# Performance work log

Measured on AMD Instinct MI355X. Metric: run time of the kernel, lower is better.

The kernel has to match this reference:

```python
import jax, jax.numpy as jnp
import numpy as np

B, C, D, H, W = 4, 128, 16, 16, 16
INNER = 64  # channels // reduction


def setup_inputs() -> dict:
    key = jax.random.key(0)
    ks = jax.random.split(key, 4)
    s = 0.02
    return {
        "x": jax.random.normal(ks[0], (B, C, D, H, W), dtype=jnp.float32),
        "Wq": jax.random.normal(ks[1], (INNER, C), dtype=jnp.float32) * s,
        "bq": jnp.zeros((INNER,), dtype=jnp.float32),
        "Wk": jax.random.normal(ks[2], (INNER, C), dtype=jnp.float32) * s,
        "bk": jnp.zeros((INNER,), dtype=jnp.float32),
        "Wv": jax.random.normal(ks[3], (C, C), dtype=jnp.float32) * s,
        "bv": jnp.zeros((C,), dtype=jnp.float32),
        "gamma": jnp.zeros((1,), dtype=jnp.float32),
    }


def reference(x, Wq, bq, Wk, bk, Wv, bv, gamma):
    b, c, d, h, w = x.shape
    n = d * h * w
    inner = Wq.shape[0]
    scale = inner ** (-0.5)
    xf = x.reshape(b, c, n)  # flatten spatial dims
    # 1x1 Conv3d == per-position channel matmul
    q = jnp.einsum('oc,bcn->bon', Wq, xf) + bq[None, :, None]  # [B, inner, N]
    k = jnp.einsum('oc,bcn->bon', Wk, xf) + bk[None, :, None]  # [B, inner, N]
    v = jnp.einsum('oc,bcn->bon', Wv, xf) + bv[None, :, None]  # [B, C, N]
    # attn[b, n, m] = softmax_m(q[:, :, n] . k[:, :, m] * scale)
    attn = jax.nn.softmax(jnp.einsum('bon,bom->bnm', q, k) * scale, axis=-1)
    # out = v @ attn^T  -> out[b, c, n] = sum_m v[b, c, m] * attn[b, n, m]
    out = jnp.einsum('bcm,bnm->bcn', v, attn).reshape(b, c, d, h, w)
    return x + gamma[0] * out
```

## Files before the change

kernel.cpp:

```cpp
#include <hip/hip_runtime.h>
#include <cstdint>

#define B_ 4
#define C_ 128
#define INNER_ 64
#define N_ 4096
#define S_ 4
#define KEYS_PER_BLOCK (N_ / S_)
#define KT 64
#define NT (KEYS_PER_BLOCK / KT)

typedef __attribute__((ext_vector_type(8))) short short8;
typedef __attribute__((ext_vector_type(4))) float f32x4;

typedef const __attribute__((address_space(1))) void* gp_t;
typedef __attribute__((address_space(3))) void* lp_t;

__device__ __forceinline__ short f2bf(float f) {
  unsigned u = __builtin_bit_cast(unsigned, f);
  unsigned r = (u + 0x7FFFu + ((u >> 16) & 1u)) >> 16;
  return (short)r;
}

__global__ __launch_bounds__(256) void pack_kernel(
    const float* __restrict__ Wq, const float* __restrict__ bq,
    const float* __restrict__ Wk, const float* __restrict__ bk,
    const float* __restrict__ Wv, const float* __restrict__ bv,
    short* __restrict__ wp, float* __restrict__ bp)
{
  const int idx = blockIdx.x * 256 + threadIdx.x;
  const int o = idx >> 7, c = idx & 127;
  float v;
  if (o < 64)       v = Wq[o * C_ + c];
  else if (o < 128) v = Wk[(o - 64) * C_ + c];
  else              v = Wv[(o - 128) * C_ + c];
  wp[idx] = f2bf(v);
  if (c == 0)
    bp[o] = (o < 64) ? bq[o] : (o < 128) ? bk[o - 64] : bv[o - 128];
}

__global__ __launch_bounds__(256) void qkv_kernel(
    const float* __restrict__ x, const short* __restrict__ wp,
    const float* __restrict__ bp,
    short* __restrict__ qb, short* __restrict__ kb, short* __restrict__ vb)
{
  __shared__ short xT[16 * 136];
  const int tid = threadIdx.x;
  const int b   = blockIdx.x >> 8;
  const int n0  = (blockIdx.x & 255) << 4;

  const float* xb = x + (size_t)b * C_ * N_ + n0;
  for (int i = tid; i < 512; i += 256) {
    const int c = i >> 2, seg = i & 3;
    const float4 v = *(const float4*)&xb[(size_t)c * N_ + seg * 4];
    xT[(seg * 4 + 0) * 136 + c] = f2bf(v.x);
    xT[(seg * 4 + 1) * 136 + c] = f2bf(v.y);
    xT[(seg * 4 + 2) * 136 + c] = f2bf(v.z);
    xT[(seg * 4 + 3) * 136 + c] = f2bf(v.w);
  }
  __syncthreads();

  const int w = tid >> 6, lane = tid & 63, quad = lane >> 4, l16 = lane & 15;

#pragma unroll
  for (int oi = 0; oi < 4; ++oi) {
    const int ot = w + oi * 4;
    const int o  = ot * 16 + l16;

    short8 bf[4];
#pragma unroll
    for (int ks = 0; ks < 4; ++ks)
      bf[ks] = *(const short8*)&wp[(size_t)o * 128 + ks * 32 + quad * 8];

    f32x4 acc = (f32x4){0.f, 0.f, 0.f, 0.f};
#pragma unroll
    for (int ks = 0; ks < 4; ++ks) {
      short8 af = *(const short8*)&xT[l16 * 136 + ks * 32 + quad * 8];
      acc = __builtin_amdgcn_mfma_f32_16x16x32_bf16(af, bf[ks], acc, 0, 0, 0);
    }

    const float bias = bp[o];
#pragma unroll
    for (int r = 0; r < 4; ++r) {
      const int n = n0 + quad * 4 + r;
      const short sv = f2bf(acc[r] + bias);
      if (o < 64)       qb[((size_t)b * N_ + n) * 64 + o] = sv;
      else if (o < 128) kb[((size_t)b * N_ + n) * 64 + (o - 64)] = sv;
      else              vb[((size_t)b * C_ + (o - 128)) * N_ + n] = sv;
    }
  }
}

__global__ __launch_bounds__(256) void attn_kernel(
    const short* __restrict__ qb, const short* __restrict__ kb,
    const short* __restrict__ vb,
    float* __restrict__ Opart, float* __restrict__ lbuf)
{
  __shared__ short kbuf[2][4096];
  __shared__ short vbuf[2][8192];
  __shared__ short parena[4][2048];

  const int tid = threadIdx.x;
  const int bid = blockIdx.x;
  const int b   = bid >> 7;
  const int qt  = (bid >> 2) & 31;
  const int s   = bid & 3;
  const int m0  = qt << 7;
  const int w   = tid >> 6, lane = tid & 63, quad = lane >> 4, l16 = lane & 15;
  const int rbase = m0 + w * 32;

  short* pw = parena[w];

  const float kS = 0.125f * 1.44269504088896340736f;

  short8 qa[2][2];
#pragma unroll
  for (int mt = 0; mt < 2; ++mt)
#pragma unroll
    for (int kk = 0; kk < 2; ++kk)
      qa[mt][kk] = *(const short8*)&qb[((size_t)b * N_ + rbase + mt * 16 + l16) * 64 + kk * 32 + quad * 8];

  float lsum[2][4];
#pragma unroll
  for (int mt = 0; mt < 2; ++mt)
#pragma unroll
    for (int r = 0; r < 4; ++r) lsum[mt][r] = 0.f;
  f32x4 accO[2][8];
#pragma unroll
  for (int mt = 0; mt < 2; ++mt)
#pragma unroll
    for (int ct = 0; ct < 8; ++ct) accO[mt][ct] = (f32x4){0.f, 0.f, 0.f, 0.f};

  const int kslice = s * KEYS_PER_BLOCK;

  auto dma_tile = [&](int kt, int d) {
    const int kbase = kslice + kt * KT;
#pragma unroll
    for (int t = 0; t < 2; ++t) {
      const int p = (w * 2 + t) * 64 + lane;
      const int key = p >> 3, jm = (p & 7) ^ (key & 7);
      const short* src = kb + (((size_t)b * N_ + kbase + key) << 6) + jm * 8;
      __builtin_amdgcn_global_load_lds((gp_t)src, (lp_t)&kbuf[d][(w * 2 + t) * 512], 16, 0, 0);
    }
#pragma unroll
    for (int t = 0; t < 4; ++t) {
      const int p = (w * 4 + t) * 64 + lane;
      const int ch = p >> 3, jm = (p & 7) ^ (ch & 7);
      const short* src = vb + ((size_t)b * C_ + ch) * N_ + kbase + jm * 8;
      __builtin_amdgcn_global_load_lds((gp_t)src, (lp_t)&vbuf[d][(w * 4 + t) * 512], 16, 0, 0);
    }
  };

  dma_tile(0, 0);

  for (int kt = 0; kt < NT; ++kt) {
    __syncthreads();
    if (kt + 1 < NT) dma_tile(kt + 1, (kt + 1) & 1);
    const int d = kt & 1;

#pragma unroll
    for (int ct = 0; ct < 4; ++ct) {
      short8 kf[2];
#pragma unroll
      for (int kk = 0; kk < 2; ++kk)
        kf[kk] = *(const short8*)&kbuf[d][((ct * 16 + l16) << 6) + (((kk * 4 + quad) ^ (l16 & 7)) << 3)];
      f32x4 s0 = (f32x4){0.f, 0.f, 0.f, 0.f};
      f32x4 s1 = (f32x4){0.f, 0.f, 0.f, 0.f};
      s0 = __builtin_amdgcn_mfma_f32_16x16x32_bf16(qa[0][0], kf[0], s0, 0, 0, 0);
      s0 = __builtin_amdgcn_mfma_f32_16x16x32_bf16(qa[0][1], kf[1], s0, 0, 0, 0);
      s1 = __builtin_amdgcn_mfma_f32_16x16x32_bf16(qa[1][0], kf[0], s1, 0, 0, 0);
      s1 = __builtin_amdgcn_mfma_f32_16x16x32_bf16(qa[1][1], kf[1], s1, 0, 0, 0);

      const int jp = ct * 2 + (l16 >> 3);
      const int off = l16 & 7;
#pragma unroll
      for (int r = 0; r < 4; ++r) {
        const int row0 = quad * 4 + r;
        const float p0 = exp2f(s0[r] * kS);
        lsum[0][r] += p0;
        pw[(row0 << 6) + ((jp ^ (row0 & 7)) << 3) + off] = f2bf(p0);
        const float p1 = exp2f(s1[r] * kS);
        lsum[1][r] += p1;
        pw[((16 + row0) << 6) + ((jp ^ (row0 & 7)) << 3) + off] = f2bf(p1);
      }
    }

#pragma unroll
    for (int ks = 0; ks < 2; ++ks) {
      short8 pa0 = *(const short8*)&pw[(l16 << 6) + (((ks * 4 + quad) ^ (l16 & 7)) << 3)];
      short8 pa1 = *(const short8*)&pw[((16 + l16) << 6) + (((ks * 4 + quad) ^ (l16 & 7)) << 3)];
#pragma unroll
      for (int ct = 0; ct < 8; ++ct) {
        short8 vf = *(const short8*)&vbuf[d][((ct * 16 + l16) << 6) + (((ks * 4 + quad) ^ (l16 & 7)) << 3)];
        accO[0][ct] = __builtin_amdgcn_mfma_f32_16x16x32_bf16(pa0, vf, accO[0][ct], 0, 0, 0);
        accO[1][ct] = __builtin_amdgcn_mfma_f32_16x16x32_bf16(pa1, vf, accO[1][ct], 0, 0, 0);
      }
    }
  }

#pragma unroll
  for (int mt = 0; mt < 2; ++mt) {
#pragma unroll
    for (int r = 0; r < 4; ++r) {
      lsum[mt][r] += __shfl_xor(lsum[mt][r], 1);
      lsum[mt][r] += __shfl_xor(lsum[mt][r], 2);
      lsum[mt][r] += __shfl_xor(lsum[mt][r], 4);
      lsum[mt][r] += __shfl_xor(lsum[mt][r], 8);
    }
    if (l16 == 0) {
#pragma unroll
      for (int r = 0; r < 4; ++r)
        lbuf[((size_t)b * S_ + s) * N_ + rbase + mt * 16 + quad * 4 + r] = lsum[mt][r];
    }
#pragma unroll
    for (int ct = 0; ct < 8; ++ct) {
#pragma unroll
      for (int r = 0; r < 4; ++r) {
        const int n = rbase + mt * 16 + quad * 4 + r;
        Opart[(((size_t)b * S_ + s) * N_ + n) * C_ + ct * 16 + l16] = accO[mt][ct][r];
      }
    }
  }
}

__global__ __launch_bounds__(256) void combine_kernel(
    const float* __restrict__ x, const float* __restrict__ gamma,
    const float* __restrict__ Opart, const float* __restrict__ lbuf,
    float* __restrict__ out)
{
  __shared__ float Of[32][133];
  __shared__ float Linv[32];

  const int t  = threadIdx.x;
  const int b  = blockIdx.x >> 7;
  const int n0 = (blockIdx.x & 127) << 5;

  const int c4 = (t & 31) * 4, nrow = t >> 5;
#pragma unroll
  for (int np = 0; np < 4; ++np) {
    const int n = np * 8 + nrow;
    f32x4 acc = (f32x4){0.f, 0.f, 0.f, 0.f};
#pragma unroll
    for (int sp = 0; sp < S_; ++sp) {
      const f32x4 v = *(const f32x4*)&Opart[(((size_t)b * S_ + sp) * N_ + n0 + n) * C_ + c4];
      acc += v;
    }
    Of[n][c4 + 0] = acc[0];
    Of[n][c4 + 1] = acc[1];
    Of[n][c4 + 2] = acc[2];
    Of[n][c4 + 3] = acc[3];
  }
  if (t < 32) {
    float L = 0.f;
#pragma unroll
    for (int sp = 0; sp < S_; ++sp) L += lbuf[((size_t)b * S_ + sp) * N_ + n0 + t];
    Linv[t] = 1.f / L;
  }
  __syncthreads();

  const float g = gamma[0];
  const int nn = t & 31, cb = t >> 5;
#pragma unroll
  for (int cp = 0; cp < 16; ++cp) {
    const int c = cp * 8 + cb;
    const size_t idx = ((size_t)b * C_ + c) * N_ + n0 + nn;
    out[idx] = x[idx] + g * Of[nn][c] * Linv[nn];
  }
}

extern "C" void kernel_launch(void* const* d_in, const int* in_sizes, int n_in,
                              void* d_out, int out_size, void* d_ws, size_t ws_size,
                              hipStream_t stream) {
  const float* x     = (const float*)d_in[0];
  const float* Wq    = (const float*)d_in[1];
  const float* bq    = (const float*)d_in[2];
  const float* Wk    = (const float*)d_in[3];
  const float* bk    = (const float*)d_in[4];
  const float* Wv    = (const float*)d_in[5];
  const float* bv    = (const float*)d_in[6];
  const float* gamma = (const float*)d_in[7];
  float* out = (float*)d_out;

  short* qb = (short*)d_ws;
  short* kb = qb + (size_t)B_ * N_ * INNER_;
  short* vb = kb + (size_t)B_ * N_ * INNER_;
  float* Opart = (float*)(vb + (size_t)B_ * C_ * N_);
  float* lbuf  = Opart + (size_t)B_ * S_ * N_ * C_;
  float* bp    = lbuf + (size_t)B_ * S_ * N_;
  short* wp    = (short*)(bp + 256);

  pack_kernel<<<128, 256, 0, stream>>>(Wq, bq, Wk, bk, Wv, bv, wp, bp);
  qkv_kernel<<<B_ * (N_ / 16), 256, 0, stream>>>(x, wp, bp, qb, kb, vb);
  attn_kernel<<<B_ * (N_ / 128) * S_, 256, 0, stream>>>(qb, kb, vb, Opart, lbuf);
  combine_kernel<<<B_ * (N_ / 32), 256, 0, stream>>>(x, gamma, Opart, lbuf, out);
}
```

Measured before the change: 143.9 us.

## Rework attention pipeline: register-resident P, bf16 partials, more key splits

The attention kernel now computes transposed scores (K·Q) so the bf16 probabilities stay in registers and feed 16x16x16 MFMAs directly, which removes the LDS round trip for P. Key splits double from 4 to 8 and launch bounds request 3 blocks per CU for more parallelism. Partial outputs are stored as bf16 in channel-major layout, so combine can read them vectorized, and a separate kernel precomputes the inverse row sums. The QKV projection now handles 32 positions per block and stages results in LDS for coalesced 16-byte stores. The costs are lower precision in the partial sums, twice as much partial data to reduce, and one extra kernel launch.

```diff
diff --git a/kernel.cpp b/kernel.cpp
--- a/kernel.cpp
+++ b/kernel.cpp
@@ -5,12 +5,13 @@
 #define C_ 128
 #define INNER_ 64
 #define N_ 4096
-#define S_ 4
+#define S_ 8
 #define KEYS_PER_BLOCK (N_ / S_)
 #define KT 64
 #define NT (KEYS_PER_BLOCK / KT)
 
 typedef __attribute__((ext_vector_type(8))) short short8;
+typedef __attribute__((ext_vector_type(4))) short bf16x4;
 typedef __attribute__((ext_vector_type(4))) float f32x4;
 
 typedef const __attribute__((address_space(1))) void* gp_t;
@@ -20,6 +21,22 @@
   unsigned u = __builtin_bit_cast(unsigned, f);
   unsigned r = (u + 0x7FFFu + ((u >> 16) & 1u)) >> 16;
   return (short)r;
+}
+__device__ __forceinline__ float bf2f(short s) {
+  return __builtin_bit_cast(float, ((unsigned)(unsigned short)s) << 16);
+}
+
+__device__ __forceinline__ f32x4 mfma16(bf16x4 a, bf16x4 b, f32x4 c) {
+#if __has_builtin(__builtin_amdgcn_mfma_f32_16x16x16bf16_1k)
+  return __builtin_amdgcn_mfma_f32_16x16x16bf16_1k(a, b, c, 0, 0, 0);
+#elif __has_builtin(__builtin_amdgcn_mfma_f32_16x16x16_bf16)
+  return __builtin_amdgcn_mfma_f32_16x16x16_bf16(a, b, c, 0, 0, 0);
+#else
+  f32x4 d;
+  asm volatile("v_mfma_f32_16x16x16_bf16 %0, %1, %2, %3"
+               : "=v"(d) : "v"(a), "v"(b), "v"(c));
+  return d;
+#endif
 }
 
 __global__ __launch_bounds__(256) void pack_kernel(
@@ -42,16 +59,20 @@
 __global__ __launch_bounds__(256) void qkv_kernel(
     const float* __restrict__ x, const short* __restrict__ wp,
     const float* __restrict__ bp,
-    short* __restrict__ qb, short* __restrict__ kb, short* __restrict__ vb)
-{
-  __shared__ short xT[16 * 136];
+    short* __restrict__ qg, short* __restrict__ kg, short* __restrict__ vg)
+{
+  __shared__ short xT[32 * 136];
+  __shared__ short outb[256 * 40];
+  __shared__ float biasL[256];
+
   const int tid = threadIdx.x;
-  const int b   = blockIdx.x >> 8;
-  const int n0  = (blockIdx.x & 255) << 4;
-
+  const int b   = blockIdx.x >> 7;
+  const int n0  = (blockIdx.x & 127) << 5;
+
+  biasL[tid] = bp[tid];
   const float* xb = x + (size_t)b * C_ * N_ + n0;
-  for (int i = tid; i < 512; i += 256) {
-    const int c = i >> 2, seg = i & 3;
+  for (int i = tid; i < 1024; i += 256) {
+    const int c = i >> 3, seg = i & 7;
     const float4 v = *(const float4*)&xb[(size_t)c * N_ + seg * 4];
     xT[(seg * 4 + 0) * 136 + c] = f2bf(v.x);
     xT[(seg * 4 + 1) * 136 + c] = f2bf(v.y);
@@ -62,55 +83,96 @@
 
   const int w = tid >> 6, lane = tid & 63, quad = lane >> 4, l16 = lane & 15;
 
-#pragma unroll
-  for (int oi = 0; oi < 4; ++oi) {
-    const int ot = w + oi * 4;
-    const int o  = ot * 16 + l16;
-
-    short8 bf[4];
-#pragma unroll
-    for (int ks = 0; ks < 4; ++ks)
-      bf[ks] = *(const short8*)&wp[(size_t)o * 128 + ks * 32 + quad * 8];
-
-    f32x4 acc = (f32x4){0.f, 0.f, 0.f, 0.f};
-#pragma unroll
-    for (int ks = 0; ks < 4; ++ks) {
-      short8 af = *(const short8*)&xT[l16 * 136 + ks * 32 + quad * 8];
-      acc = __builtin_amdgcn_mfma_f32_16x16x32_bf16(af, bf[ks], acc, 0, 0, 0);
-    }
-
-    const float bias = bp[o];
-#pragma unroll
-    for (int r = 0; r < 4; ++r) {
-      const int n = n0 + quad * 4 + r;
-      const short sv = f2bf(acc[r] + bias);
-      if (o < 64)       qb[((size_t)b * N_ + n) * 64 + o] = sv;
-      else if (o < 128) kb[((size_t)b * N_ + n) * 64 + (o - 64)] = sv;
-      else              vb[((size_t)b * C_ + (o - 128)) * N_ + n] = sv;
-    }
-  }
-}
-
-__global__ __launch_bounds__(256) void attn_kernel(
+  short8 xf[2][4];
+#pragma unroll
+  for (int nt = 0; nt < 2; ++nt)
+#pragma unroll
+    for (int kk = 0; kk < 4; ++kk)
+      xf[nt][kk] = *(const short8*)&xT[(nt * 16 + l16) * 136 + kk * 32 + quad * 8];
+
+  if (w < 2) {
+    const int obase = w * 64;
+#pragma unroll
+    for (int ot = 0; ot < 4; ++ot) {
+      const int o = obase + ot * 16 + l16;
+      short8 wf[4];
+#pragma unroll
+      for (int kk = 0; kk < 4; ++kk)
+        wf[kk] = *(const short8*)&wp[(size_t)o * 128 + kk * 32 + quad * 8];
+      const float bias = biasL[o];
+#pragma unroll
+      for (int nt = 0; nt < 2; ++nt) {
+        f32x4 acc = (f32x4){0.f, 0.f, 0.f, 0.f};
+#pragma unroll
+        for (int kk = 0; kk < 4; ++kk)
+          acc = __builtin_amdgcn_mfma_f32_16x16x32_bf16(xf[nt][kk], wf[kk], acc, 0, 0, 0);
+#pragma unroll
+        for (int r = 0; r < 4; ++r)
+          outb[o * 40 + nt * 16 + quad * 4 + r] = f2bf(acc[r] + bias);
+      }
+    }
+  } else {
+    const int ob2 = (w - 2) * 64;
+#pragma unroll
+    for (int ot = 0; ot < 4; ++ot) {
+      const int orow = 128 + ob2 + ot * 16 + l16;
+      short8 wf[4];
+#pragma unroll
+      for (int kk = 0; kk < 4; ++kk)
+        wf[kk] = *(const short8*)&wp[(size_t)orow * 128 + kk * 32 + quad * 8];
+#pragma unroll
+      for (int nt = 0; nt < 2; ++nt) {
+        f32x4 acc = (f32x4){0.f, 0.f, 0.f, 0.f};
+#pragma unroll
+        for (int kk = 0; kk < 4; ++kk)
+          acc = __builtin_amdgcn_mfma_f32_16x16x32_bf16(wf[kk], xf[nt][kk], acc, 0, 0, 0);
+#pragma unroll
+        for (int r = 0; r < 4; ++r) {
+          const int o_r = 128 + ob2 + ot * 16 + quad * 4 + r;
+          outb[o_r * 40 + nt * 16 + l16] = f2bf(acc[r] + biasL[o_r]);
+        }
+      }
+    }
+  }
+  __syncthreads();
+
+  {
+    const int n = tid >> 3, oc = tid & 7;
+    short8 qv, kv;
+#pragma unroll
+    for (int j = 0; j < 8; ++j) {
+      qv[j] = outb[(oc * 8 + j) * 40 + n];
+      kv[j] = outb[(64 + oc * 8 + j) * 40 + n];
+    }
+    *(short8*)&qg[(((size_t)b * N_ + n0 + n) << 6) + oc * 8] = qv;
+    *(short8*)&kg[(((size_t)b * N_ + n0 + n) << 6) + oc * 8] = kv;
+#pragma unroll
+    for (int rep = 0; rep < 2; ++rep) {
+      const int idx2 = tid + rep * 256;
+      const int orel = idx2 >> 2, nc = idx2 & 3;
+      const short8 vv = *(const short8*)&outb[(128 + orel) * 40 + nc * 8];
+      *(short8*)&vg[(((size_t)b * C_ + orel) << 12) + n0 + nc * 8] = vv;
+    }
+  }
+}
+
+__global__ __launch_bounds__(256, 3) void attn_kernel(
     const short* __restrict__ qb, const short* __restrict__ kb,
     const short* __restrict__ vb,
-    float* __restrict__ Opart, float* __restrict__ lbuf)
+    short* __restrict__ Opart, float* __restrict__ lbuf)
 {
   __shared__ short kbuf[2][4096];
   __shared__ short vbuf[2][8192];
-  __shared__ short parena[4][2048];
 
   const int tid = threadIdx.x;
   const int bid = blockIdx.x;
-  const int b   = bid >> 7;
-  const int qt  = (bid >> 2) & 31;
-  const int s   = bid & 3;
+  const int b   = bid >> 8;
+  const int qt  = (bid >> 3) & 31;
+  const int s   = bid & 7;
   const int m0  = qt << 7;
   const int w   = tid >> 6, lane = tid & 63, quad = lane >> 4, l16 = lane & 15;
   const int rbase = m0 + w * 32;
 
-  short* pw = parena[w];
-
   const float kS = 0.125f * 1.44269504088896340736f;
 
   short8 qa[2][2];
@@ -120,16 +182,12 @@
     for (int kk = 0; kk < 2; ++kk)
       qa[mt][kk] = *(const short8*)&qb[((size_t)b * N_ + rbase + mt * 16 + l16) * 64 + kk * 32 + quad * 8];
 
-  float lsum[2][4];
-#pragma unroll
-  for (int mt = 0; mt < 2; ++mt)
-#pragma unroll
-    for (int r = 0; r < 4; ++r) lsum[mt][r] = 0.f;
-  f32x4 accO[2][8];
-#pragma unroll
-  for (int mt = 0; mt < 2; ++mt)
-#pragma unroll
-    for (int ct = 0; ct < 8; ++ct) accO[mt][ct] = (f32x4){0.f, 0.f, 0.f, 0.f};
+  float lsum[2] = {0.f, 0.f};
+  f32x4 accO[8][2];
+#pragma unroll
+  for (int vt = 0; vt < 8; ++vt)
+#pragma unroll
+    for (int mt = 0; mt < 2; ++mt) accO[vt][mt] = (f32x4){0.f, 0.f, 0.f, 0.f};
 
   const int kslice = s * KEYS_PER_BLOCK;
 
@@ -158,114 +216,107 @@
     if (kt + 1 < NT) dma_tile(kt + 1, (kt + 1) & 1);
     const int d = kt & 1;
 
+    bf16x4 pbf[4][2];
 #pragma unroll
     for (int ct = 0; ct < 4; ++ct) {
-      short8 kf[2];
-#pragma unroll
-      for (int kk = 0; kk < 2; ++kk)
-        kf[kk] = *(const short8*)&kbuf[d][((ct * 16 + l16) << 6) + (((kk * 4 + quad) ^ (l16 & 7)) << 3)];
-      f32x4 s0 = (f32x4){0.f, 0.f, 0.f, 0.f};
-      f32x4 s1 = (f32x4){0.f, 0.f, 0.f, 0.f};
-      s0 = __builtin_amdgcn_mfma_f32_16x16x32_bf16(qa[0][0], kf[0], s0, 0, 0, 0);
-      s0 = __builtin_amdgcn_mfma_f32_16x16x32_bf16(qa[0][1], kf[1], s0, 0, 0, 0);
-      s1 = __builtin_amdgcn_mfma_f32_16x16x32_bf16(qa[1][0], kf[0], s1, 0, 0, 0);
-      s1 = __builtin_amdgcn_mfma_f32_16x16x32_bf16(qa[1][1], kf[1], s1, 0, 0, 0);
-
-      const int jp = ct * 2 + (l16 >> 3);
-      const int off = l16 & 7;
+      const short8 kf0 = *(const short8*)&kbuf[d][((ct * 16 + l16) << 6) + ((quad ^ (l16 & 7)) << 3)];
+      const short8 kf1 = *(const short8*)&kbuf[d][((ct * 16 + l16) << 6) + (((4 + quad) ^ (l16 & 7)) << 3)];
+#pragma unroll
+      for (int mt = 0; mt < 2; ++mt) {
+        f32x4 st = (f32x4){0.f, 0.f, 0.f, 0.f};
+        st = __builtin_amdgcn_mfma_f32_16x16x32_bf16(kf0, qa[mt][0], st, 0, 0, 0);
+        st = __builtin_amdgcn_mfma_f32_16x16x32_bf16(kf1, qa[mt][1], st, 0, 0, 0);
+        bf16x4 p4;
+#pragma unroll
+        for (int r = 0; r < 4; ++r) {
+          const float p = exp2f(st[r] * kS);
+          lsum[mt] += p;
+          p4[r] = f2bf(p);
+        }
+        pbf[ct][mt] = p4;
+      }
+    }
+
+#pragma unroll
+    for (int vt = 0; vt < 8; ++vt) {
+#pragma unroll
+      for (int ct = 0; ct < 4; ++ct) {
+        const int chunk = ct * 2 + (quad >> 1);
+        const bf16x4 vf = *(const bf16x4*)&vbuf[d][((vt * 16 + l16) << 6) +
+                              ((chunk ^ (l16 & 7)) << 3) + ((quad & 1) << 2)];
+        accO[vt][0] = mfma16(vf, pbf[ct][0], accO[vt][0]);
+        accO[vt][1] = mfma16(vf, pbf[ct][1], accO[vt][1]);
+      }
+    }
+  }
+
+#pragma unroll
+  for (int mt = 0; mt < 2; ++mt) {
+    lsum[mt] += __shfl_xor(lsum[mt], 16);
+    lsum[mt] += __shfl_xor(lsum[mt], 32);
+  }
+  if (quad == 0) {
+#pragma unroll
+    for (int mt = 0; mt < 2; ++mt)
+      lbuf[((size_t)b * S_ + s) * N_ + rbase + mt * 16 + l16] = lsum[mt];
+  }
+#pragma unroll
+  for (int vt = 0; vt < 8; ++vt) {
+#pragma unroll
+    for (int mt = 0; mt < 2; ++mt) {
 #pragma unroll
       for (int r = 0; r < 4; ++r) {
-        const int row0 = quad * 4 + r;
-        const float p0 = exp2f(s0[r] * kS);
-        lsum[0][r] += p0;
-        pw[(row0 << 6) + ((jp ^ (row0 & 7)) << 3) + off] = f2bf(p0);
-        const float p1 = exp2f(s1[r] * kS);
-        lsum[1][r] += p1;
-        pw[((16 + row0) << 6) + ((jp ^ (row0 & 7)) << 3) + off] = f2bf(p1);
-      }
-    }
-
-#pragma unroll
-    for (int ks = 0; ks < 2; ++ks) {
-      short8 pa0 = *(const short8*)&pw[(l16 << 6) + (((ks * 4 + quad) ^ (l16 & 7)) << 3)];
-      short8 pa1 = *(const short8*)&pw[((16 + l16) << 6) + (((ks * 4 + quad) ^ (l16 & 7)) << 3)];
-#pragma unroll
-      for (int ct = 0; ct < 8; ++ct) {
-        short8 vf = *(const short8*)&vbuf[d][((ct * 16 + l16) << 6) + (((ks * 4 + quad) ^ (l16 & 7)) << 3)];
-        accO[0][ct] = __builtin_amdgcn_mfma_f32_16x16x32_bf16(pa0, vf, accO[0][ct], 0, 0, 0);
-        accO[1][ct] = __builtin_amdgcn_mfma_f32_16x16x32_bf16(pa1, vf, accO[1][ct], 0, 0, 0);
-      }
-    }
-  }
-
-#pragma unroll
-  for (int mt = 0; mt < 2; ++mt) {
-#pragma unroll
-    for (int r = 0; r < 4; ++r) {
-      lsum[mt][r] += __shfl_xor(lsum[mt][r], 1);
-      lsum[mt][r] += __shfl_xor(lsum[mt][r], 2);
-      lsum[mt][r] += __shfl_xor(lsum[mt][r], 4);
-      lsum[mt][r] += __shfl_xor(lsum[mt][r], 8);
-    }
-    if (l16 == 0) {
-#pragma unroll
-      for (int r = 0; r < 4; ++r)
-        lbuf[((size_t)b * S_ + s) * N_ + rbase + mt * 16 + quad * 4 + r] = lsum[mt][r];
-    }
-#pragma unroll
-    for (int ct = 0; ct < 8; ++ct) {
-#pragma unroll
-      for (int r = 0; r < 4; ++r) {
-        const int n = rbase + mt * 16 + quad * 4 + r;
-        Opart[(((size_t)b * S_ + s) * N_ + n) * C_ + ct * 16 + l16] = accO[mt][ct][r];
-      }
-    }
-  }
+        const int ch = vt * 16 + quad * 4 + r;
+        Opart[(((size_t)b * S_ + s) * C_ + ch) * N_ + rbase + mt * 16 + l16] =
+            f2bf(accO[vt][mt][r]);
+      }
+    }
+  }
+}
+
+__global__ __launch_bounds__(256) void linv_kernel(
+    const float* __restrict__ lbuf, float* __restrict__ linv)
+{
+  const int idx = blockIdx.x * 256 + threadIdx.x;
+  const int b = idx >> 12, n = idx & (N_ - 1);
+  float L = 0.f;
+#pragma unroll
+  for (int s = 0; s < S_; ++s) L += lbuf[((size_t)b * S_ + s) * N_ + n];
+  linv[idx] = 1.f / L;
 }
 
 __global__ __launch_bounds__(256) void combine_kernel(
     const float* __restrict__ x, const float* __restrict__ gamma,
-    const float* __restrict__ Opart, const float* __restrict__ lbuf,
+    const short* __restrict__ Opart, const float* __restrict__ linv,
     float* __restrict__ out)
 {
-  __shared__ float Of[32][133];
-  __shared__ float Linv[32];
-
-  const int t  = threadIdx.x;
-  const int b  = blockIdx.x >> 7;
-  const int n0 = (blockIdx.x & 127) << 5;
-
-  const int c4 = (t & 31) * 4, nrow = t >> 5;
-#pragma unroll
-  for (int np = 0; np < 4; ++np) {
-    const int n = np * 8 + nrow;
-    f32x4 acc = (f32x4){0.f, 0.f, 0.f, 0.f};
-#pragma unroll
-    for (int sp = 0; sp < S_; ++sp) {
-      const f32x4 v = *(const f32x4*)&Opart[(((size_t)b * S_ + sp) * N_ + n0 + n) * C_ + c4];
-      acc += v;
-    }
-    Of[n][c4 + 0] = acc[0];
-    Of[n][c4 + 1] = acc[1];
-    Of[n][c4 + 2] = acc[2];
-    Of[n][c4 + 3] = acc[3];
-  }
-  if (t < 32) {
-    float L = 0.f;
-#pragma unroll
-    for (int sp = 0; sp < S_; ++sp) L += lbuf[((size_t)b * S_ + sp) * N_ + n0 + t];
-    Linv[t] = 1.f / L;
-  }
-  __syncthreads();
-
+  const int idx = blockIdx.x * 256 + threadIdx.x;
+  const int n = (idx & 511) << 3;
+  const int c = (idx >> 9) & 127;
+  const int b = idx >> 16;
+
+  float acc[8];
+#pragma unroll
+  for (int j = 0; j < 8; ++j) acc[j] = 0.f;
+#pragma unroll
+  for (int s = 0; s < S_; ++s) {
+    const short8 o8 = *(const short8*)&Opart[(((size_t)b * S_ + s) * C_ + c) * N_ + n];
+#pragma unroll
+    for (int j = 0; j < 8; ++j) acc[j] += bf2f(o8[j]);
+  }
+  const float4 li0 = *(const float4*)&linv[((size_t)b << 12) + n];
+  const float4 li1 = *(const float4*)&linv[((size_t)b << 12) + n + 4];
   const float g = gamma[0];
-  const int nn = t & 31, cb = t >> 5;
-#pragma unroll
-  for (int cp = 0; cp < 16; ++cp) {
-    const int c = cp * 8 + cb;
-    const size_t idx = ((size_t)b * C_ + c) * N_ + n0 + nn;
-    out[idx] = x[idx] + g * Of[nn][c] * Linv[nn];
-  }
+  const size_t xi = ((size_t)b * C_ + c) * N_ + n;
+  const float4 x0 = *(const float4*)&x[xi];
+  const float4 x1 = *(const float4*)&x[xi + 4];
+  float4 o0, o1;
+  o0.x = x0.x + g * acc[0] * li0.x;  o0.y = x0.y + g * acc[1] * li0.y;
+  o0.z = x0.z + g * acc[2] * li0.z;  o0.w = x0.w + g * acc[3] * li0.w;
+  o1.x = x1.x + g * acc[4] * li1.x;  o1.y = x1.y + g * acc[5] * li1.y;
+  o1.z = x1.z + g * acc[6] * li1.z;  o1.w = x1.w + g * acc[7] * li1.w;
+  *(float4*)&out[xi] = o0;
+  *(float4*)&out[xi + 4] = o1;
 }
 
 extern "C" void kernel_launch(void* const* d_in, const int* in_sizes, int n_in,
@@ -284,13 +335,15 @@
   short* qb = (short*)d_ws;
   short* kb = qb + (size_t)B_ * N_ * INNER_;
   short* vb = kb + (size_t)B_ * N_ * INNER_;
-  float* Opart = (float*)(vb + (size_t)B_ * C_ * N_);
-  float* lbuf  = Opart + (size_t)B_ * S_ * N_ * C_;
-  float* bp    = lbuf + (size_t)B_ * S_ * N_;
+  short* Opart = vb + (size_t)B_ * C_ * N_;
+  float* lbuf  = (float*)(Opart + (size_t)B_ * S_ * C_ * N_);
+  float* linv  = lbuf + (size_t)B_ * S_ * N_;
+  float* bp    = linv + (size_t)B_ * N_;
   short* wp    = (short*)(bp + 256);
 
   pack_kernel<<<128, 256, 0, stream>>>(Wq, bq, Wk, bk, Wv, bv, wp, bp);
-  qkv_kernel<<<B_ * (N_ / 16), 256, 0, stream>>>(x, wp, bp, qb, kb, vb);
+  qkv_kernel<<<B_ * (N_ / 32), 256, 0, stream>>>(x, wp, bp, qb, kb, vb);
   attn_kernel<<<B_ * (N_ / 128) * S_, 256, 0, stream>>>(qb, kb, vb, Opart, lbuf);
-  combine_kernel<<<B_ * (N_ / 32), 256, 0, stream>>>(x, gamma, Opart, lbuf, out);
-}
+  linv_kernel<<<(B_ * N_) / 256, 256, 0, stream>>>(lbuf, linv);
+  combine_kernel<<<(B_ * C_ * N_ / 8) / 256, 256, 0, stream>>>(x, gamma, Opart, linv, out);
+}
```

After: 134.9 us. -6.3%, faster.
